# Performance work log

Hardware: AMD Instinct MI355X
Metric: run time of the kernel (lower is better)

Reference implementation:

```python
import jax, jax.numpy as jnp
import numpy as np

D_MODEL = 1024
D_INNER = 2048
D_STATE = 16
DT_RANK = 64  # ceil(1024/16)
N_LAYERS = 4
SEQ = 4096


def setup_inputs() -> dict:
    key = jax.random.key(0)
    ks = list(jax.random.split(key, 8))
    L, d, di, n, r = N_LAYERS, D_MODEL, D_INNER, D_STATE, DT_RANK
    def rn(k, shape, scale):
        return jax.random.normal(k, shape, dtype=jnp.float32) * scale
    A_init = jnp.tile(jnp.log(jnp.arange(1, n + 1, dtype=jnp.float32))[None, None, :], (L, di, 1))
    return {
        'x': jax.random.normal(ks[0], (SEQ, d), dtype=jnp.float32),
        'pos_enc': jax.random.normal(ks[1], (SEQ, d), dtype=jnp.float32),
        'ln_g': jnp.ones((d,), jnp.float32),
        'ln_b': jnp.zeros((d,), jnp.float32),
        'innorm_g': jnp.ones((L, d), jnp.float32),
        'innorm_b': jnp.zeros((L, d), jnp.float32),
        'in_proj_w': rn(ks[2], (L, 2 * di, d), 0.02),
        'in_proj_b': jnp.zeros((L, 2 * di), jnp.float32),
        'conv_w': rn(ks[3], (L, di, 1, 3), 0.1),
        'conv_b': jnp.zeros((L, di), jnp.float32),
        'deltaBC_w': rn(ks[4], (L, r + 2 * n, di), 0.02),
        'dt_proj_w': rn(ks[5], (L, di, r), 0.02),
        'dt_proj_b': jnp.zeros((L, di), jnp.float32),
        'A_log': A_init,
        'Dp': jnp.ones((L, di), jnp.float32),
        'outnorm_g': jnp.ones((L, di), jnp.float32),
        'outnorm_b': jnp.zeros((L, di), jnp.float32),
        'out_proj_w': rn(ks[6], (L, d, di), 0.02),
        'out_proj_b': jnp.zeros((L, d), jnp.float32),
    }


def _ln(x, g, b, eps):
    mu = jnp.mean(x, axis=-1, keepdims=True)
    var = jnp.mean((x - mu) ** 2, axis=-1, keepdims=True)
    return (x - mu) * jax.lax.rsqrt(var + eps) * g + b


def _selective_scan(u, delta, A, B, C, D):
    # u, delta: [b,l,d]; A: [d,n]; B, C: [b,l,n]; D: [d]
    b, l, d = u.shape
    n = A.shape[1]
    def step(h, inputs):
        d_t, B_t, u_t, C_t = inputs          # [b,d],[b,n],[b,d],[b,n]
        dA = jnp.exp(d_t[:, :, None] * A)    # [b,d,n]
        dBu = (d_t * u_t)[:, :, None] * B_t[:, None, :]
        h = dA * h + dBu
        y = jnp.einsum('bdn,bn->bd', h, C_t)
        return h, y
    h0 = jnp.zeros((b, d, n), u.dtype)
    xs = (jnp.swapaxes(delta, 0, 1), jnp.swapaxes(B, 0, 1),
          jnp.swapaxes(u, 0, 1), jnp.swapaxes(C, 0, 1))
    _, ys = jax.lax.scan(step, h0, xs)       # ys: [l,b,d]
    return jnp.swapaxes(ys, 0, 1) + u * D


def _block(x, innorm_g, innorm_b, in_proj_w, in_proj_b, conv_w, conv_b,
           deltaBC_w, dt_proj_w, dt_proj_b, A_log, Dp, outnorm_g, outnorm_b,
           out_proj_w, out_proj_b):
    skip = x
    h = _ln(x, innorm_g, innorm_b, 1e-5)
    xz = h @ in_proj_w.T + in_proj_b
    x1, z1 = jnp.split(xz, 2, axis=-1)       # [b,s,di] each
    # depthwise conv1d, k=3, pad=1
    xc = jnp.swapaxes(x1, 1, 2)              # [b,di,s]
    xc = jax.lax.conv_general_dilated(xc, conv_w, (1,), [(1, 1)],
                                      feature_group_count=xc.shape[1],
                                      dimension_numbers=('NCH', 'OIH', 'NCH'))
    xc = xc + conv_b[None, :, None]
    u = jnp.swapaxes(xc, 1, 2)               # [b,s,di]
    # SSM
    A = -jnp.exp(A_log)
    dbc = u @ deltaBC_w.T                    # [b,s,r+2n]
    delta, B, C = jnp.split(dbc, [DT_RANK, DT_RANK + D_STATE], axis=-1)
    delta = jax.nn.softplus(delta @ dt_proj_w.T + dt_proj_b)
    y = _selective_scan(u, delta, A, B, C, Dp)
    y = _ln(y, outnorm_g, outnorm_b, 1e-5)
    out = y * jax.nn.silu(z1)
    return out @ out_proj_w.T + out_proj_b + skip


def _forward(x, pos_enc, ln_g, ln_b, innorm_g, innorm_b, in_proj_w, in_proj_b,
             conv_w, conv_b, deltaBC_w, dt_proj_w, dt_proj_b, A_log, Dp,
             outnorm_g, outnorm_b, out_proj_w, out_proj_b):
    enc = _ln(x + pos_enc, ln_g, ln_b, 1e-6)[None]  # [1,s,d]
    for i in range(N_LAYERS):
        enc = _block(enc, innorm_g[i], innorm_b[i], in_proj_w[i], in_proj_b[i],
                     conv_w[i], conv_b[i], deltaBC_w[i], dt_proj_w[i],
                     dt_proj_b[i], A_log[i], Dp[i], outnorm_g[i], outnorm_b[i],
                     out_proj_w[i], out_proj_b[i])
    return enc[0]


def reference(x, pos_enc, ln_g, ln_b, innorm_g, innorm_b, in_proj_w, in_proj_b,
              conv_w, conv_b, deltaBC_w, dt_proj_w, dt_proj_b, A_log, Dp,
              outnorm_g, outnorm_b, out_proj_w, out_proj_b):
    return _forward(x, pos_enc, ln_g, ln_b, innorm_g, innorm_b, in_proj_w,
                    in_proj_b, conv_w, conv_b, deltaBC_w, dt_proj_w, dt_proj_b,
                    A_log, Dp, outnorm_g, outnorm_b, out_proj_w, out_proj_b)
```

## Files before the change

kernel.cpp:

```cpp
#include <hip/hip_runtime.h>
#include <hip/hip_bf16.h>
#include <stdint.h>


#define SEQ     4096
#define DMODEL  1024
#define DINNER  2048
#define NSTATE  16
#define DTRANK  64
#define NLAYERS 4
#define LC      64
#define NC      64

typedef __attribute__((ext_vector_type(8))) short short8v;
typedef __attribute__((ext_vector_type(4))) float f32x4;
typedef __hip_bfloat16 bf16;

__device__ __forceinline__ float b2f(unsigned short x) {
    unsigned int u = ((unsigned int)x) << 16;
    return __builtin_bit_cast(float, u);
}

__device__ __forceinline__ void gld16(const void* gsrc, void* ldst) {
    __builtin_amdgcn_global_load_lds(
        (const __attribute__((address_space(1))) void*)gsrc,
        (__attribute__((address_space(3))) void*)ldst, 16, 0, 0);
}

__device__ __forceinline__ float block_sum(float v, float* red, int nwaves) {
    #pragma unroll
    for (int o = 32; o > 0; o >>= 1) v += __shfl_down(v, o, 64);
    int lane = threadIdx.x & 63, w = threadIdx.x >> 6;
    __syncthreads();
    if (lane == 0) red[w] = v;
    __syncthreads();
    float s = red[0];
    for (int i = 1; i < nwaves; i++) s += red[i];
    return s;
}

template<int WIDTH, typename OutT>
__global__ void ln_kernel(const float* __restrict__ X, const float* __restrict__ X2,
                          const float* __restrict__ g, const float* __restrict__ bta,
                          OutT* __restrict__ out, float eps) {
    constexpr int E = WIDTH / 256;
    __shared__ float red[4];
    int s = blockIdx.x, tid = threadIdx.x;
    size_t base = (size_t)s * WIDTH;
    float v[E]; float sum = 0.f;
    #pragma unroll
    for (int i = 0; i < E; i++) {
        int c = tid + i * 256;
        float t = X[base + c];
        if (X2) t += X2[base + c];
        v[i] = t; sum += t;
    }
    float mu = block_sum(sum, red, 4) * (1.f / WIDTH);
    float sq = 0.f;
    #pragma unroll
    for (int i = 0; i < E; i++) { float d = v[i] - mu; sq += d * d; }
    float var = block_sum(sq, red, 4) * (1.f / WIDTH);
    float rstd = rsqrtf(var + eps);
    #pragma unroll
    for (int i = 0; i < E; i++) {
        int c = tid + i * 256;
        float r = (v[i] - mu) * rstd * g[c] + bta[c];
        out[base + c] = (OutT)r;
    }
}

__global__ void outnorm_silu_kernel(const float* __restrict__ y, const bf16* __restrict__ xz,
                                    const float* __restrict__ g, const float* __restrict__ bta,
                                    bf16* __restrict__ p_bf, float eps) {
    constexpr int WIDTH = DINNER, E = WIDTH / 256;
    __shared__ float red[4];
    int s = blockIdx.x, tid = threadIdx.x;
    size_t base = (size_t)s * WIDTH;
    const unsigned short* xzu = (const unsigned short*)xz;
    float v[E]; float sum = 0.f;
    #pragma unroll
    for (int i = 0; i < E; i++) { int c = tid + i * 256; v[i] = y[base + c]; sum += v[i]; }
    float mu = block_sum(sum, red, 4) * (1.f / WIDTH);
    float sq = 0.f;
    #pragma unroll
    for (int i = 0; i < E; i++) { float d = v[i] - mu; sq += d * d; }
    float var = block_sum(sq, red, 4) * (1.f / WIDTH);
    float rstd = rsqrtf(var + eps);
    #pragma unroll
    for (int i = 0; i < E; i++) {
        int c = tid + i * 256;
        float ln = (v[i] - mu) * rstd * g[c] + bta[c];
        float z = b2f(xzu[(size_t)s * (2 * DINNER) + DINNER + c]);
        float sig = 1.f / (1.f + __expf(-z));
        p_bf[base + c] = __float2bfloat16(ln * (z * sig));
    }
}

__global__ void conv_kernel(const bf16* __restrict__ xz, const float* __restrict__ cw,
                            const float* __restrict__ cb, bf16* __restrict__ u_bf) {
    int t = blockIdx.x * 256 + threadIdx.x;
    int s = t >> 9, c = (t & 511) * 4;
    size_t row = (size_t)s * (2 * DINNER);
    const unsigned short* xp = (const unsigned short*)xz;
    ushort4 z4 = {0, 0, 0, 0};
    ushort4 v0 = *(const ushort4*)(xp + row + c);
    ushort4 vm = (s > 0)       ? *(const ushort4*)(xp + row - 2 * DINNER + c) : z4;
    ushort4 vp = (s < SEQ - 1) ? *(const ushort4*)(xp + row + 2 * DINNER + c) : z4;
    unsigned short o[4];
    float x0[4] = {b2f(v0.x), b2f(v0.y), b2f(v0.z), b2f(v0.w)};
    float xm[4] = {b2f(vm.x), b2f(vm.y), b2f(vm.z), b2f(vm.w)};
    float xp4[4] = {b2f(vp.x), b2f(vp.y), b2f(vp.z), b2f(vp.w)};
    #pragma unroll
    for (int i = 0; i < 4; i++) {
        int ch = c + i;
        float u = cw[ch * 3 + 0] * xm[i] + cw[ch * 3 + 1] * x0[i]
                + cw[ch * 3 + 2] * xp4[i] + cb[ch];
        o[i] = __builtin_bit_cast(unsigned short, __float2bfloat16(u));
    }
    *(ushort4*)((unsigned short*)u_bf + (size_t)s * DINNER + c) = {o[0], o[1], o[2], o[3]};
}

#define CN0 (2 * DINNER * DMODEL)
#define CN1 (DMODEL * DINNER)
#define CN2 (96 * DINNER)
#define CN3 (DINNER * DTRANK)
__global__ void cvt_all_kernel(const float* __restrict__ w0, const float* __restrict__ w1,
                               const float* __restrict__ w2, const float* __restrict__ w3,
                               bf16* __restrict__ o0, bf16* __restrict__ o1,
                               bf16* __restrict__ o2, bf16* __restrict__ o3) {
    size_t i = (size_t)(blockIdx.x * 256 + threadIdx.x) * 4;
    const float* src; bf16* dst;
    if (i < CN0)                   { src = w0; dst = o0; }
    else if (i < CN0 + CN1)        { src = w1; dst = o1; i -= CN0; }
    else if (i < CN0 + CN1 + CN2)  { src = w2; dst = o2; i -= CN0 + CN1; }
    else                           { src = w3; dst = o3; i -= CN0 + CN1 + CN2; }
    float4 v = *(const float4*)(src + i);
    __hip_bfloat162 t0, t1;
    t0.x = __float2bfloat16(v.x); t0.y = __float2bfloat16(v.y);
    t1.x = __float2bfloat16(v.z); t1.y = __float2bfloat16(v.w);
    __hip_bfloat162* o = (__hip_bfloat162*)(dst + i);
    o[0] = t0; o[1] = t1;
}

template<int MODE>
__global__ __launch_bounds__(256, 3)
void mfma_gemm(const bf16* __restrict__ A, int lda,
               const bf16* __restrict__ W, int ldw,
               const float* __restrict__ bias,
               float* __restrict__ C, int ldc,
               const float* __restrict__ res,
               bf16* __restrict__ Cbf,
               int M, int N, int K) {
    __shared__ __attribute__((aligned(16))) short sA[128][64];
    __shared__ __attribute__((aligned(16))) short sB[128][64];
    int tid = threadIdx.x;
    int lane = tid & 63, w = tid >> 6;
    int wm = w >> 1, wn = w & 1;
    int m0 = blockIdx.x * 128, n0 = blockIdx.y * 128;
    int r16 = lane & 15, quad = lane >> 4;

    if (MODE == 1) {
        int kz = blockIdx.z;
        A += (size_t)kz * K;
        W += (size_t)kz * K;
        C += (size_t)kz * M * 96;
    }

    f32x4 acc[4][4] = {};

    for (int k0 = 0; k0 < K; k0 += 64) {
        __syncthreads();
        #pragma unroll
        for (int j = 0; j < 4; j++) {
            int idx = j * 256 + tid;
            int row = idx >> 3;
            int csrc = (idx & 7) ^ (row & 7);
            gld16(A + (size_t)(m0 + row) * lda + k0 + csrc * 8,
                  (char*)&sA[0][0] + j * 4096 + w * 1024);
            int nr = n0 + row; if (nr > N - 1) nr = N - 1;
            gld16(W + (size_t)nr * ldw + k0 + csrc * 8,
                  (char*)&sB[0][0] + j * 4096 + w * 1024);
        }
        __syncthreads();
        #pragma unroll
        for (int s = 0; s < 2; s++) {
            short8v aF[4], bF[4];
            #pragma unroll
            for (int mi = 0; mi < 4; mi++)
                aF[mi] = *(const short8v*)
                    &sA[wm * 64 + mi * 16 + r16][((s * 4 + quad) ^ (r16 & 7)) * 8];
            #pragma unroll
            for (int ni = 0; ni < 4; ni++)
                bF[ni] = *(const short8v*)
                    &sB[wn * 64 + ni * 16 + r16][((s * 4 + quad) ^ (r16 & 7)) * 8];
            #pragma unroll
            for (int mi = 0; mi < 4; mi++)
                #pragma unroll
                for (int ni = 0; ni < 4; ni++)
                    acc[mi][ni] = __builtin_amdgcn_mfma_f32_16x16x32_bf16(
                        aF[mi], bF[ni], acc[mi][ni], 0, 0, 0);
        }
    }

    #pragma unroll
    for (int mi = 0; mi < 4; mi++) {
        #pragma unroll
        for (int ni = 0; ni < 4; ni++) {
            f32x4 a = acc[mi][ni];
            int col = n0 + wn * 64 + ni * 16 + r16;
            int rbase = m0 + wm * 64 + mi * 16 + quad * 4;
            #pragma unroll
            for (int r = 0; r < 4; r++) {
                int row = rbase + r;
                float v = a[r];
                if (MODE == 0 || MODE == 2 || MODE == 3) v += bias[col];
                if (MODE == 2) v = (v > 20.f) ? v : log1pf(__expf(v));
                if (MODE == 3) v += res[(size_t)row * ldc + col];
                if (MODE == 1) {
                    if (col < 96) C[(size_t)row * 96 + col] = v;
                } else if (MODE == 0) {
                    Cbf[(size_t)row * ldc + col] = __float2bfloat16(v);
                } else {
                    C[(size_t)row * ldc + col] = v;
                }
            }
        }
    }
}

__global__ void reduce_dbc_kernel(const float* __restrict__ p, float* __restrict__ dbc,
                                  bf16* __restrict__ dbc_bf) {
    int i = blockIdx.x * 256 + threadIdx.x;
    const int SP = SEQ * 96;
    float v = p[i] + p[i + SP] + p[i + 2 * SP] + p[i + 3 * SP];
    dbc[i] = v;
    int row = i / 96, c = i - row * 96;
    if (c < DTRANK) dbc_bf[(size_t)row * DTRANK + c] = __float2bfloat16(v);
}

__device__ __forceinline__ bool a_is_neg_integers(const float* a) {
    bool fast = true;
    #pragma unroll
    for (int n = 0; n < NSTATE; n++)
        fast = fast && (__builtin_fabsf(a[n] + (float)(n + 1)) < 1e-3f * (n + 1));
    return fast;
}

__global__ __launch_bounds__(256)
void scan1_kernel(const float* __restrict__ delta, const bf16* __restrict__ u,
                  const float* __restrict__ dbc, const float* __restrict__ A_log,
                  float* __restrict__ h_end, float* __restrict__ dsum) {
    int k = blockIdx.x, d = blockIdx.y * 256 + threadIdx.x;
    int s0 = k * LC;
    float a[NSTATE];
    #pragma unroll
    for (int n = 0; n < NSTATE; n++) a[n] = -__expf(A_log[(size_t)d * NSTATE + n]);
    bool fast = a_is_neg_integers(a);
    const float* dp = delta + (size_t)s0 * DINNER + d;
    const unsigned short* up = (const unsigned short*)u + (size_t)s0 * DINNER + d;
    const float* br = dbc + (size_t)s0 * 96 + DTRANK;
    float h[NSTATE] = {};
    float ds = 0.f;
    if (fast) {
        #pragma unroll 2
        for (int r = 0; r < LC; r++) {
            float dl = *dp;
            float uu = b2f(*up);
            float4 b0 = *(const float4*)(br);
            float4 b1 = *(const float4*)(br + 4);
            float4 b2 = *(const float4*)(br + 8);
            float4 b3 = *(const float4*)(br + 12);
            float Bv[NSTATE] = {b0.x, b0.y, b0.z, b0.w, b1.x, b1.y, b1.z, b1.w,
                                b2.x, b2.y, b2.z, b2.w, b3.x, b3.y, b3.z, b3.w};
            ds += dl;
            float du = dl * uu;
            float g = __expf(-dl);
            float fac = 1.f;
            #pragma unroll
            for (int n = 0; n < NSTATE; n++) {
                fac *= g;
                h[n] = fac * h[n] + du * Bv[n];
            }
            dp += DINNER; up += DINNER; br += 96;
        }
    } else {
        #pragma unroll 2
        for (int r = 0; r < LC; r++) {
            float dl = *dp;
            float uu = b2f(*up);
            float4 b0 = *(const float4*)(br);
            float4 b1 = *(const float4*)(br + 4);
            float4 b2 = *(const float4*)(br + 8);
            float4 b3 = *(const float4*)(br + 12);
            float Bv[NSTATE] = {b0.x, b0.y, b0.z, b0.w, b1.x, b1.y, b1.z, b1.w,
                                b2.x, b2.y, b2.z, b2.w, b3.x, b3.y, b3.z, b3.w};
            ds += dl;
            float du = dl * uu;
            #pragma unroll
            for (int n = 0; n < NSTATE; n++)
                h[n] = __expf(dl * a[n]) * h[n] + du * Bv[n];
            dp += DINNER; up += DINNER; br += 96;
        }
    }
    #pragma unroll
    for (int n = 0; n < NSTATE; n++)
        h_end[((size_t)k * NSTATE + n) * DINNER + d] = h[n];
    dsum[(size_t)k * DINNER + d] = ds;
}

__global__ void scan2_kernel(const float* __restrict__ A_log, const float* __restrict__ dsum,
                             const float* __restrict__ h_end, float* __restrict__ hinit) {
    int id = blockIdx.x * 256 + threadIdx.x;
    int d = id & (DINNER - 1), n = id >> 11;
    float a = -__expf(A_log[(size_t)d * NSTATE + n]);
    float h = 0.f;
    #pragma unroll 4
    for (int k = 0; k < NC; k++) {
        size_t off = ((size_t)k * NSTATE + n) * DINNER + d;
        hinit[off] = h;
        h = __expf(a * dsum[(size_t)k * DINNER + d]) * h + h_end[off];
    }
}

__global__ __launch_bounds__(256)
void scan3_kernel(float* __restrict__ delta_y, const bf16* __restrict__ u,
                  const float* __restrict__ dbc, const float* __restrict__ A_log,
                  const float* __restrict__ Dp, const float* __restrict__ hinit) {
    int k = blockIdx.x, d = blockIdx.y * 256 + threadIdx.x;
    int s0 = k * LC;
    float a[NSTATE];
    #pragma unroll
    for (int n = 0; n < NSTATE; n++) a[n] = -__expf(A_log[(size_t)d * NSTATE + n]);
    bool fast = a_is_neg_integers(a);
    float h[NSTATE];
    #pragma unroll
    for (int n = 0; n < NSTATE; n++)
        h[n] = hinit[((size_t)k * NSTATE + n) * DINNER + d];
    float dpv = Dp[d];
    float* dp = delta_y + (size_t)s0 * DINNER + d;
    const unsigned short* up = (const unsigned short*)u + (size_t)s0 * DINNER + d;
    const float* br = dbc + (size_t)s0 * 96 + DTRANK;
    if (fast) {
        #pragma unroll 2
        for (int r = 0; r < LC; r++) {
            float dl = *dp;
            float uu = b2f(*up);
            float4 b0 = *(const float4*)(br);
            float4 b1 = *(const float4*)(br + 4);
            float4 b2 = *(const float4*)(br + 8);
            float4 b3 = *(const float4*)(br + 12);
            float4 c0 = *(const float4*)(br + 16);
            float4 c1 = *(const float4*)(br + 20);
            float4 c2 = *(const float4*)(br + 24);
            float4 c3 = *(const float4*)(br + 28);
            float Bv[NSTATE] = {b0.x, b0.y, b0.z, b0.w, b1.x, b1.y, b1.z, b1.w,
                                b2.x, b2.y, b2.z, b2.w, b3.x, b3.y, b3.z, b3.w};
            float Cv[NSTATE] = {c0.x, c0.y, c0.z, c0.w, c1.x, c1.y, c1.z, c1.w,
                                c2.x, c2.y, c2.z, c2.w, c3.x, c3.y, c3.z, c3.w};
            float du = dl * uu;
            float g = __expf(-dl);
            float y = uu * dpv;
            float fac = 1.f;
            #pragma unroll
            for (int n = 0; n < NSTATE; n++) {
                fac *= g;
                h[n] = fac * h[n] + du * Bv[n];
                y += h[n] * Cv[n];
            }
            *dp = y;
            dp += DINNER; up += DINNER; br += 96;
        }
    } else {
        #pragma unroll 2
        for (int r = 0; r < LC; r++) {
            float dl = *dp;
            float uu = b2f(*up);
            float4 b0 = *(const float4*)(br);
            float4 b1 = *(const float4*)(br + 4);
            float4 b2 = *(const float4*)(br + 8);
            float4 b3 = *(const float4*)(br + 12);
            float4 c0 = *(const float4*)(br + 16);
            float4 c1 = *(const float4*)(br + 20);
            float4 c2 = *(const float4*)(br + 24);
            float4 c3 = *(const float4*)(br + 28);
            float Bv[NSTATE] = {b0.x, b0.y, b0.z, b0.w, b1.x, b1.y, b1.z, b1.w,
                                b2.x, b2.y, b2.z, b2.w, b3.x, b3.y, b3.z, b3.w};
            float Cv[NSTATE] = {c0.x, c0.y, c0.z, c0.w, c1.x, c1.y, c1.z, c1.w,
                                c2.x, c2.y, c2.z, c2.w, c3.x, c3.y, c3.z, c3.w};
            float du = dl * uu;
            float y = uu * dpv;
            #pragma unroll
            for (int n = 0; n < NSTATE; n++) {
                h[n] = __expf(dl * a[n]) * h[n] + du * Bv[n];
                y += h[n] * Cv[n];
            }
            *dp = y;
            dp += DINNER; up += DINNER; br += 96;
        }
    }
}

extern "C" void kernel_launch(void* const* d_in, const int* in_sizes, int n_in,
                              void* d_out, int out_size, void* d_ws, size_t ws_size,
                              hipStream_t stream) {
    const float* x         = (const float*)d_in[0];
    const float* pos       = (const float*)d_in[1];
    const float* ln_g      = (const float*)d_in[2];
    const float* ln_b      = (const float*)d_in[3];
    const float* innorm_g  = (const float*)d_in[4];
    const float* innorm_b  = (const float*)d_in[5];
    const float* in_proj_w = (const float*)d_in[6];
    const float* in_proj_b = (const float*)d_in[7];
    const float* conv_w    = (const float*)d_in[8];
    const float* conv_b    = (const float*)d_in[9];
    const float* deltaBC_w = (const float*)d_in[10];
    const float* dt_proj_w = (const float*)d_in[11];
    const float* dt_proj_b = (const float*)d_in[12];
    const float* A_log     = (const float*)d_in[13];
    const float* Dp        = (const float*)d_in[14];
    const float* outnorm_g = (const float*)d_in[15];
    const float* outnorm_b = (const float*)d_in[16];
    const float* out_proj_w= (const float*)d_in[17];
    const float* out_proj_b= (const float*)d_in[18];

    float* enc = (float*)d_out;
    char* ws = (char*)d_ws;
    const size_t MB = 1024 * 1024;
    bf16*  h_bf   = (bf16*) (ws + 0);
    bf16*  p_bf   = (bf16*) (ws + 0);
    bf16*  xz_bf  = (bf16*) (ws + 16 * MB);
    float* dlt    = (float*)(ws + 48 * MB);
    float* dbcp   = (float*)(ws + 48 * MB);
    bf16*  u_bf   = (bf16*) (ws + 80 * MB);
    float* dbc    = (float*)(ws + 96 * MB);
    bf16*  dbc_bf = (bf16*) (ws + 98 * MB);
    float* h_end  = (float*)(ws + 99 * MB);
    float* hinit  = (float*)(ws + 107 * MB);
    float* dsum   = (float*)(ws + 115 * MB);
    bf16*  w_in   = (bf16*) (ws + 116 * MB);
    bf16*  w_dbc  = (bf16*) (ws + 124 * MB);
    bf16*  w_dt   = (bf16*) (ws + 125 * MB);
    bf16*  w_out  = (bf16*) (ws + 126 * MB);

    ln_kernel<DMODEL, float><<<SEQ, 256, 0, stream>>>(x, pos, ln_g, ln_b, enc, 1e-6f);

    for (int L = 0; L < NLAYERS; L++) {
        const float* Al = A_log + (size_t)L * DINNER * NSTATE;
        cvt_all_kernel<<<(CN0 + CN1 + CN2 + CN3) / 1024, 256, 0, stream>>>(
            in_proj_w + (size_t)L * CN0, out_proj_w + (size_t)L * CN1,
            deltaBC_w + (size_t)L * CN2, dt_proj_w + (size_t)L * CN3,
            w_in, w_out, w_dbc, w_dt);

        ln_kernel<DMODEL, bf16><<<SEQ, 256, 0, stream>>>(enc, nullptr, innorm_g + L * DMODEL,
                                                         innorm_b + L * DMODEL, h_bf, 1e-5f);
        mfma_gemm<0><<<dim3(32, 32), 256, 0, stream>>>(
            h_bf, DMODEL, w_in, DMODEL, in_proj_b + (size_t)L * 2 * DINNER,
            nullptr, 2 * DINNER, nullptr, xz_bf, SEQ, 2 * DINNER, DMODEL);
        conv_kernel<<<(SEQ * 512) / 256, 256, 0, stream>>>(
            xz_bf, conv_w + (size_t)L * DINNER * 3, conv_b + L * DINNER, u_bf);
        mfma_gemm<1><<<dim3(32, 1, 4), 256, 0, stream>>>(
            u_bf, DINNER, w_dbc, DINNER, nullptr,
            dbcp, 96, nullptr, nullptr, SEQ, 96, 512);
        reduce_dbc_kernel<<<(SEQ * 96) / 256, 256, 0, stream>>>(dbcp, dbc, dbc_bf);
        mfma_gemm<2><<<dim3(32, 16), 256, 0, stream>>>(
            dbc_bf, DTRANK, w_dt, DTRANK, dt_proj_b + L * DINNER,
            dlt, DINNER, nullptr, nullptr, SEQ, DINNER, DTRANK);
        scan1_kernel<<<dim3(NC, DINNER / 256), 256, 0, stream>>>(dlt, u_bf, dbc, Al, h_end, dsum);
        scan2_kernel<<<(DINNER * NSTATE) / 256, 256, 0, stream>>>(Al, dsum, h_end, hinit);
        scan3_kernel<<<dim3(NC, DINNER / 256), 256, 0, stream>>>(dlt, u_bf, dbc, Al,
                                                                 Dp + L * DINNER, hinit);
        outnorm_silu_kernel<<<SEQ, 256, 0, stream>>>(dlt, xz_bf, outnorm_g + L * DINNER,
                                                     outnorm_b + L * DINNER, p_bf, 1e-5f);
        mfma_gemm<3><<<dim3(32, 8), 256, 0, stream>>>(
            p_bf, DINNER, w_out, DINNER, out_proj_b + L * DMODEL,
            enc, DMODEL, enc, nullptr, SEQ, DMODEL, DINNER);
    }
}
```

Before: 1.093 ms.

## Fuse three scan phases into one cooperative kernel and hoist weight conversion

Merges the chunked selective scan's three kernels (local chunk scan, cross-chunk prefix, final output pass) into one cooperative kernel that uses grid-wide syncs between phases. It also converts all four layers' weights to bf16 in a single launch before the layer loop instead of once per layer, which needs a larger workspace. The aim is to cut launch overhead and per-layer conversion passes. In exchange, the whole 512-block grid must be co-resident, and the prefix phase leaves most blocks idle between the two grid barriers.

New measurement: 1.604 ms. 46.7% more time.

```diff
diff --git a/kernel.cpp b/kernel.cpp
--- a/kernel.cpp
+++ b/kernel.cpp
@@ -1,6 +1,9 @@
 #include <hip/hip_runtime.h>
 #include <hip/hip_bf16.h>
+#include <hip/hip_cooperative_groups.h>
 #include <stdint.h>
+
+namespace cg = cooperative_groups;
 
 
 #define SEQ     4096
@@ -124,16 +127,20 @@
 #define CN1 (DMODEL * DINNER)
 #define CN2 (96 * DINNER)
 #define CN3 (DINNER * DTRANK)
-__global__ void cvt_all_kernel(const float* __restrict__ w0, const float* __restrict__ w1,
-                               const float* __restrict__ w2, const float* __restrict__ w3,
-                               bf16* __restrict__ o0, bf16* __restrict__ o1,
-                               bf16* __restrict__ o2, bf16* __restrict__ o3) {
+#define S0 (4 * CN0)
+#define S1 (4 * CN1)
+#define S2 (4 * CN2)
+#define S3 (4 * CN3)
+__global__ void cvt4_kernel(const float* __restrict__ w0, const float* __restrict__ w1,
+                            const float* __restrict__ w2, const float* __restrict__ w3,
+                            bf16* __restrict__ o0, bf16* __restrict__ o1,
+                            bf16* __restrict__ o2, bf16* __restrict__ o3) {
     size_t i = (size_t)(blockIdx.x * 256 + threadIdx.x) * 4;
     const float* src; bf16* dst;
-    if (i < CN0)                   { src = w0; dst = o0; }
-    else if (i < CN0 + CN1)        { src = w1; dst = o1; i -= CN0; }
-    else if (i < CN0 + CN1 + CN2)  { src = w2; dst = o2; i -= CN0 + CN1; }
-    else                           { src = w3; dst = o3; i -= CN0 + CN1 + CN2; }
+    if (i < S0)                { src = w0; dst = o0; }
+    else if (i < S0 + S1)      { src = w1; dst = o1; i -= S0; }
+    else if (i < S0 + S1 + S2) { src = w2; dst = o2; i -= S0 + S1; }
+    else                       { src = w3; dst = o3; i -= S0 + S1 + S2; }
     float4 v = *(const float4*)(src + i);
     __hip_bfloat162 t0, t1;
     t0.x = __float2bfloat16(v.x); t0.y = __float2bfloat16(v.y);
@@ -247,155 +254,160 @@
 }
 
 __global__ __launch_bounds__(256)
-void scan1_kernel(const float* __restrict__ delta, const bf16* __restrict__ u,
-                  const float* __restrict__ dbc, const float* __restrict__ A_log,
-                  float* __restrict__ h_end, float* __restrict__ dsum) {
-    int k = blockIdx.x, d = blockIdx.y * 256 + threadIdx.x;
+void scan_fused_kernel(float* __restrict__ delta_y, const bf16* __restrict__ u,
+                       const float* __restrict__ dbc, const float* __restrict__ A_log,
+                       const float* __restrict__ Dp,
+                       float* __restrict__ h_end, float* __restrict__ dsum,
+                       float* __restrict__ hinit) {
+    cg::grid_group grid = cg::this_grid();
+    int k = blockIdx.x, tid = threadIdx.x;
+    int d = blockIdx.y * 256 + tid;
     int s0 = k * LC;
     float a[NSTATE];
     #pragma unroll
     for (int n = 0; n < NSTATE; n++) a[n] = -__expf(A_log[(size_t)d * NSTATE + n]);
     bool fast = a_is_neg_integers(a);
-    const float* dp = delta + (size_t)s0 * DINNER + d;
-    const unsigned short* up = (const unsigned short*)u + (size_t)s0 * DINNER + d;
-    const float* br = dbc + (size_t)s0 * 96 + DTRANK;
-    float h[NSTATE] = {};
-    float ds = 0.f;
-    if (fast) {
-        #pragma unroll 2
-        for (int r = 0; r < LC; r++) {
-            float dl = *dp;
-            float uu = b2f(*up);
-            float4 b0 = *(const float4*)(br);
-            float4 b1 = *(const float4*)(br + 4);
-            float4 b2 = *(const float4*)(br + 8);
-            float4 b3 = *(const float4*)(br + 12);
-            float Bv[NSTATE] = {b0.x, b0.y, b0.z, b0.w, b1.x, b1.y, b1.z, b1.w,
-                                b2.x, b2.y, b2.z, b2.w, b3.x, b3.y, b3.z, b3.w};
-            ds += dl;
-            float du = dl * uu;
-            float g = __expf(-dl);
-            float fac = 1.f;
-            #pragma unroll
-            for (int n = 0; n < NSTATE; n++) {
-                fac *= g;
-                h[n] = fac * h[n] + du * Bv[n];
-            }
-            dp += DINNER; up += DINNER; br += 96;
-        }
-    } else {
-        #pragma unroll 2
-        for (int r = 0; r < LC; r++) {
-            float dl = *dp;
-            float uu = b2f(*up);
-            float4 b0 = *(const float4*)(br);
-            float4 b1 = *(const float4*)(br + 4);
-            float4 b2 = *(const float4*)(br + 8);
-            float4 b3 = *(const float4*)(br + 12);
-            float Bv[NSTATE] = {b0.x, b0.y, b0.z, b0.w, b1.x, b1.y, b1.z, b1.w,
-                                b2.x, b2.y, b2.z, b2.w, b3.x, b3.y, b3.z, b3.w};
-            ds += dl;
-            float du = dl * uu;
-            #pragma unroll
-            for (int n = 0; n < NSTATE; n++)
-                h[n] = __expf(dl * a[n]) * h[n] + du * Bv[n];
-            dp += DINNER; up += DINNER; br += 96;
-        }
-    }
-    #pragma unroll
-    for (int n = 0; n < NSTATE; n++)
-        h_end[((size_t)k * NSTATE + n) * DINNER + d] = h[n];
-    dsum[(size_t)k * DINNER + d] = ds;
-}
-
-__global__ void scan2_kernel(const float* __restrict__ A_log, const float* __restrict__ dsum,
-                             const float* __restrict__ h_end, float* __restrict__ hinit) {
-    int id = blockIdx.x * 256 + threadIdx.x;
-    int d = id & (DINNER - 1), n = id >> 11;
-    float a = -__expf(A_log[(size_t)d * NSTATE + n]);
-    float h = 0.f;
-    #pragma unroll 4
-    for (int k = 0; k < NC; k++) {
-        size_t off = ((size_t)k * NSTATE + n) * DINNER + d;
-        hinit[off] = h;
-        h = __expf(a * dsum[(size_t)k * DINNER + d]) * h + h_end[off];
-    }
-}
-
-__global__ __launch_bounds__(256)
-void scan3_kernel(float* __restrict__ delta_y, const bf16* __restrict__ u,
-                  const float* __restrict__ dbc, const float* __restrict__ A_log,
-                  const float* __restrict__ Dp, const float* __restrict__ hinit) {
-    int k = blockIdx.x, d = blockIdx.y * 256 + threadIdx.x;
-    int s0 = k * LC;
-    float a[NSTATE];
-    #pragma unroll
-    for (int n = 0; n < NSTATE; n++) a[n] = -__expf(A_log[(size_t)d * NSTATE + n]);
-    bool fast = a_is_neg_integers(a);
-    float h[NSTATE];
-    #pragma unroll
-    for (int n = 0; n < NSTATE; n++)
-        h[n] = hinit[((size_t)k * NSTATE + n) * DINNER + d];
     float dpv = Dp[d];
-    float* dp = delta_y + (size_t)s0 * DINNER + d;
-    const unsigned short* up = (const unsigned short*)u + (size_t)s0 * DINNER + d;
-    const float* br = dbc + (size_t)s0 * 96 + DTRANK;
-    if (fast) {
-        #pragma unroll 2
-        for (int r = 0; r < LC; r++) {
-            float dl = *dp;
-            float uu = b2f(*up);
-            float4 b0 = *(const float4*)(br);
-            float4 b1 = *(const float4*)(br + 4);
-            float4 b2 = *(const float4*)(br + 8);
-            float4 b3 = *(const float4*)(br + 12);
-            float4 c0 = *(const float4*)(br + 16);
-            float4 c1 = *(const float4*)(br + 20);
-            float4 c2 = *(const float4*)(br + 24);
-            float4 c3 = *(const float4*)(br + 28);
-            float Bv[NSTATE] = {b0.x, b0.y, b0.z, b0.w, b1.x, b1.y, b1.z, b1.w,
-                                b2.x, b2.y, b2.z, b2.w, b3.x, b3.y, b3.z, b3.w};
-            float Cv[NSTATE] = {c0.x, c0.y, c0.z, c0.w, c1.x, c1.y, c1.z, c1.w,
-                                c2.x, c2.y, c2.z, c2.w, c3.x, c3.y, c3.z, c3.w};
-            float du = dl * uu;
-            float g = __expf(-dl);
-            float y = uu * dpv;
-            float fac = 1.f;
-            #pragma unroll
-            for (int n = 0; n < NSTATE; n++) {
-                fac *= g;
-                h[n] = fac * h[n] + du * Bv[n];
-                y += h[n] * Cv[n];
-            }
-            *dp = y;
-            dp += DINNER; up += DINNER; br += 96;
-        }
-    } else {
-        #pragma unroll 2
-        for (int r = 0; r < LC; r++) {
-            float dl = *dp;
-            float uu = b2f(*up);
-            float4 b0 = *(const float4*)(br);
-            float4 b1 = *(const float4*)(br + 4);
-            float4 b2 = *(const float4*)(br + 8);
-            float4 b3 = *(const float4*)(br + 12);
-            float4 c0 = *(const float4*)(br + 16);
-            float4 c1 = *(const float4*)(br + 20);
-            float4 c2 = *(const float4*)(br + 24);
-            float4 c3 = *(const float4*)(br + 28);
-            float Bv[NSTATE] = {b0.x, b0.y, b0.z, b0.w, b1.x, b1.y, b1.z, b1.w,
-                                b2.x, b2.y, b2.z, b2.w, b3.x, b3.y, b3.z, b3.w};
-            float Cv[NSTATE] = {c0.x, c0.y, c0.z, c0.w, c1.x, c1.y, c1.z, c1.w,
-                                c2.x, c2.y, c2.z, c2.w, c3.x, c3.y, c3.z, c3.w};
-            float du = dl * uu;
-            float y = uu * dpv;
-            #pragma unroll
-            for (int n = 0; n < NSTATE; n++) {
-                h[n] = __expf(dl * a[n]) * h[n] + du * Bv[n];
-                y += h[n] * Cv[n];
-            }
-            *dp = y;
-            dp += DINNER; up += DINNER; br += 96;
+
+    {
+        const float* dp = delta_y + (size_t)s0 * DINNER + d;
+        const unsigned short* up = (const unsigned short*)u + (size_t)s0 * DINNER + d;
+        const float* br = dbc + (size_t)s0 * 96 + DTRANK;
+        float h[NSTATE] = {};
+        float ds = 0.f;
+        if (fast) {
+            #pragma unroll 2
+            for (int r = 0; r < LC; r++) {
+                float dl = *dp;
+                float uu = b2f(*up);
+                float4 b0 = *(const float4*)(br);
+                float4 b1 = *(const float4*)(br + 4);
+                float4 b2 = *(const float4*)(br + 8);
+                float4 b3 = *(const float4*)(br + 12);
+                float Bv[NSTATE] = {b0.x, b0.y, b0.z, b0.w, b1.x, b1.y, b1.z, b1.w,
+                                    b2.x, b2.y, b2.z, b2.w, b3.x, b3.y, b3.z, b3.w};
+                ds += dl;
+                float du = dl * uu;
+                float g = __expf(-dl);
+                float fac = 1.f;
+                #pragma unroll
+                for (int n = 0; n < NSTATE; n++) {
+                    fac *= g;
+                    h[n] = fac * h[n] + du * Bv[n];
+                }
+                dp += DINNER; up += DINNER; br += 96;
+            }
+        } else {
+            #pragma unroll 2
+            for (int r = 0; r < LC; r++) {
+                float dl = *dp;
+                float uu = b2f(*up);
+                float4 b0 = *(const float4*)(br);
+                float4 b1 = *(const float4*)(br + 4);
+                float4 b2 = *(const float4*)(br + 8);
+                float4 b3 = *(const float4*)(br + 12);
+                float Bv[NSTATE] = {b0.x, b0.y, b0.z, b0.w, b1.x, b1.y, b1.z, b1.w,
+                                    b2.x, b2.y, b2.z, b2.w, b3.x, b3.y, b3.z, b3.w};
+                ds += dl;
+                float du = dl * uu;
+                #pragma unroll
+                for (int n = 0; n < NSTATE; n++)
+                    h[n] = __expf(dl * a[n]) * h[n] + du * Bv[n];
+                dp += DINNER; up += DINNER; br += 96;
+            }
+        }
+        #pragma unroll
+        for (int n = 0; n < NSTATE; n++)
+            h_end[((size_t)k * NSTATE + n) * DINNER + d] = h[n];
+        dsum[(size_t)k * DINNER + d] = ds;
+    }
+
+    grid.sync();
+
+    {
+        int bid = blockIdx.y * NC + k;
+        if (bid < (DINNER * NSTATE) / 256 / 64) {  }
+        if (bid < 128) {
+            int id = bid * 256 + tid;
+            int d2 = id & (DINNER - 1), n2 = id >> 11;
+            float a2 = -__expf(A_log[(size_t)d2 * NSTATE + n2]);
+            float h = 0.f;
+            #pragma unroll 4
+            for (int k2 = 0; k2 < NC; k2++) {
+                size_t off = ((size_t)k2 * NSTATE + n2) * DINNER + d2;
+                hinit[off] = h;
+                h = __expf(a2 * dsum[(size_t)k2 * DINNER + d2]) * h + h_end[off];
+            }
+        }
+    }
+
+    grid.sync();
+
+    {
+        float h[NSTATE];
+        #pragma unroll
+        for (int n = 0; n < NSTATE; n++)
+            h[n] = hinit[((size_t)k * NSTATE + n) * DINNER + d];
+        float* dp = delta_y + (size_t)s0 * DINNER + d;
+        const unsigned short* up = (const unsigned short*)u + (size_t)s0 * DINNER + d;
+        const float* br = dbc + (size_t)s0 * 96 + DTRANK;
+        if (fast) {
+            #pragma unroll 2
+            for (int r = 0; r < LC; r++) {
+                float dl = *dp;
+                float uu = b2f(*up);
+                float4 b0 = *(const float4*)(br);
+                float4 b1 = *(const float4*)(br + 4);
+                float4 b2 = *(const float4*)(br + 8);
+                float4 b3 = *(const float4*)(br + 12);
+                float4 c0 = *(const float4*)(br + 16);
+                float4 c1 = *(const float4*)(br + 20);
+                float4 c2 = *(const float4*)(br + 24);
+                float4 c3 = *(const float4*)(br + 28);
+                float Bv[NSTATE] = {b0.x, b0.y, b0.z, b0.w, b1.x, b1.y, b1.z, b1.w,
+                                    b2.x, b2.y, b2.z, b2.w, b3.x, b3.y, b3.z, b3.w};
+                float Cv[NSTATE] = {c0.x, c0.y, c0.z, c0.w, c1.x, c1.y, c1.z, c1.w,
+                                    c2.x, c2.y, c2.z, c2.w, c3.x, c3.y, c3.z, c3.w};
+                float du = dl * uu;
+                float g = __expf(-dl);
+                float y = uu * dpv;
+                float fac = 1.f;
+                #pragma unroll
+                for (int n = 0; n < NSTATE; n++) {
+                    fac *= g;
+                    h[n] = fac * h[n] + du * Bv[n];
+                    y += h[n] * Cv[n];
+                }
+                *dp = y;
+                dp += DINNER; up += DINNER; br += 96;
+            }
+        } else {
+            #pragma unroll 2
+            for (int r = 0; r < LC; r++) {
+                float dl = *dp;
+                float uu = b2f(*up);
+                float4 b0 = *(const float4*)(br);
+                float4 b1 = *(const float4*)(br + 4);
+                float4 b2 = *(const float4*)(br + 8);
+                float4 b3 = *(const float4*)(br + 12);
+                float4 c0 = *(const float4*)(br + 16);
+                float4 c1 = *(const float4*)(br + 20);
+                float4 c2 = *(const float4*)(br + 24);
+                float4 c3 = *(const float4*)(br + 28);
+                float Bv[NSTATE] = {b0.x, b0.y, b0.z, b0.w, b1.x, b1.y, b1.z, b1.w,
+                                    b2.x, b2.y, b2.z, b2.w, b3.x, b3.y, b3.z, b3.w};
+                float Cv[NSTATE] = {c0.x, c0.y, c0.z, c0.w, c1.x, c1.y, c1.z, c1.w,
+                                    c2.x, c2.y, c2.z, c2.w, c3.x, c3.y, c3.z, c3.w};
+                float du = dl * uu;
+                float y = uu * dpv;
+                #pragma unroll
+                for (int n = 0; n < NSTATE; n++) {
+                    h[n] = __expf(dl * a[n]) * h[n] + du * Bv[n];
+                    y += h[n] * Cv[n];
+                }
+                *dp = y;
+                dp += DINNER; up += DINNER; br += 96;
+            }
         }
     }
 }
@@ -438,41 +450,44 @@
     float* hinit  = (float*)(ws + 107 * MB);
     float* dsum   = (float*)(ws + 115 * MB);
     bf16*  w_in   = (bf16*) (ws + 116 * MB);
-    bf16*  w_dbc  = (bf16*) (ws + 124 * MB);
-    bf16*  w_dt   = (bf16*) (ws + 125 * MB);
-    bf16*  w_out  = (bf16*) (ws + 126 * MB);
+    bf16*  w_out  = (bf16*) (ws + 148 * MB);
+    bf16*  w_dbc  = (bf16*) (ws + 164 * MB);
+    bf16*  w_dt   = (bf16*) (ws + 166 * MB);
+
+    cvt4_kernel<<<(S0 + S1 + S2 + S3) / 1024, 256, 0, stream>>>(
+        in_proj_w, out_proj_w, deltaBC_w, dt_proj_w, w_in, w_out, w_dbc, w_dt);
 
     ln_kernel<DMODEL, float><<<SEQ, 256, 0, stream>>>(x, pos, ln_g, ln_b, enc, 1e-6f);
 
     for (int L = 0; L < NLAYERS; L++) {
-        const float* Al = A_log + (size_t)L * DINNER * NSTATE;
-        cvt_all_kernel<<<(CN0 + CN1 + CN2 + CN3) / 1024, 256, 0, stream>>>(
-            in_proj_w + (size_t)L * CN0, out_proj_w + (size_t)L * CN1,
-            deltaBC_w + (size_t)L * CN2, dt_proj_w + (size_t)L * CN3,
-            w_in, w_out, w_dbc, w_dt);
+        const float* Al  = A_log + (size_t)L * DINNER * NSTATE;
+        const float* Dpl = Dp + (size_t)L * DINNER;
 
         ln_kernel<DMODEL, bf16><<<SEQ, 256, 0, stream>>>(enc, nullptr, innorm_g + L * DMODEL,
                                                          innorm_b + L * DMODEL, h_bf, 1e-5f);
         mfma_gemm<0><<<dim3(32, 32), 256, 0, stream>>>(
-            h_bf, DMODEL, w_in, DMODEL, in_proj_b + (size_t)L * 2 * DINNER,
+            h_bf, DMODEL, w_in + (size_t)L * CN0, DMODEL, in_proj_b + (size_t)L * 2 * DINNER,
             nullptr, 2 * DINNER, nullptr, xz_bf, SEQ, 2 * DINNER, DMODEL);
         conv_kernel<<<(SEQ * 512) / 256, 256, 0, stream>>>(
             xz_bf, conv_w + (size_t)L * DINNER * 3, conv_b + L * DINNER, u_bf);
         mfma_gemm<1><<<dim3(32, 1, 4), 256, 0, stream>>>(
-            u_bf, DINNER, w_dbc, DINNER, nullptr,
+            u_bf, DINNER, w_dbc + (size_t)L * CN2, DINNER, nullptr,
             dbcp, 96, nullptr, nullptr, SEQ, 96, 512);
         reduce_dbc_kernel<<<(SEQ * 96) / 256, 256, 0, stream>>>(dbcp, dbc, dbc_bf);
         mfma_gemm<2><<<dim3(32, 16), 256, 0, stream>>>(
-            dbc_bf, DTRANK, w_dt, DTRANK, dt_proj_b + L * DINNER,
+            dbc_bf, DTRANK, w_dt + (size_t)L * CN3, DTRANK, dt_proj_b + L * DINNER,
             dlt, DINNER, nullptr, nullptr, SEQ, DINNER, DTRANK);
-        scan1_kernel<<<dim3(NC, DINNER / 256), 256, 0, stream>>>(dlt, u_bf, dbc, Al, h_end, dsum);
-        scan2_kernel<<<(DINNER * NSTATE) / 256, 256, 0, stream>>>(Al, dsum, h_end, hinit);
-        scan3_kernel<<<dim3(NC, DINNER / 256), 256, 0, stream>>>(dlt, u_bf, dbc, Al,
-                                                                 Dp + L * DINNER, hinit);
+        {
+            void* args[] = {(void*)&dlt, (void*)&u_bf, (void*)&dbc, (void*)&Al,
+                            (void*)&Dpl, (void*)&h_end, (void*)&dsum, (void*)&hinit};
+            hipLaunchCooperativeKernel((const void*)scan_fused_kernel,
+                                       dim3(NC, DINNER / 256), dim3(256, 1, 1),
+                                       args, 0, stream);
+        }
         outnorm_silu_kernel<<<SEQ, 256, 0, stream>>>(dlt, xz_bf, outnorm_g + L * DINNER,
                                                      outnorm_b + L * DINNER, p_bf, 1e-5f);
         mfma_gemm<3><<<dim3(32, 8), 256, 0, stream>>>(
-            p_bf, DINNER, w_out, DINNER, out_proj_b + L * DMODEL,
+            p_bf, DINNER, w_out + (size_t)L * CN1, DINNER, out_proj_b + L * DMODEL,
             enc, DMODEL, enc, nullptr, SEQ, DMODEL, DINNER);
     }
 }
```
